# Performance work log

Measured on AMD Instinct MI355X. Metric: run time of the kernel, lower is better.

The kernel has to match this reference:

```python
import jax, jax.numpy as jnp
import numpy as np

N_BUCKET, EPB, K, TAU = 4, 4, 2, 1.0
C, H = 512, 1024
E = N_BUCKET * EPB
B, T = 2, 1024

def _l2norm(v):
    # matches F.normalize(dim=-1): v / max(||v||, 1e-12)
    return v / jnp.maximum(jnp.linalg.norm(v, axis=-1, keepdims=True), 1e-12)

def setup_inputs() -> dict:
    key = jax.random.key(0)
    ks = jax.random.split(key, 8)
    s = 1.0 / np.sqrt(C).astype(np.float32)
    sh = 1.0 / np.sqrt(H).astype(np.float32)
    return {
        "x": jax.random.normal(ks[0], (B, T, C), jnp.float32),
        "op_id": jax.random.randint(ks[1], (B, T), 0, N_BUCKET),
        "expert_key": jax.random.normal(ks[2], (N_BUCKET, EPB, C), jnp.float32) * s,
        "sW1": jax.random.normal(ks[3], (C, H), jnp.float32) * s,
        "sb1": jnp.zeros((H,), jnp.float32),
        "sW2": jax.random.normal(ks[4], (H, C), jnp.float32) * sh,
        "sb2": jnp.zeros((C,), jnp.float32),
        "eW1": jax.random.normal(ks[5], (E, C, H), jnp.float32) * s,
        "eb1": jnp.zeros((E, H), jnp.float32),
        "eW2": jax.random.normal(ks[6], (E, H, C), jnp.float32) * sh,
        "eb2": jnp.zeros((E, C), jnp.float32),
        "gate_logit": jnp.float32(-2.0),
    }

def reference(x, op_id, expert_key, sW1, sb1, sW2, sb2, eW1, eb1, eW2, eb2, gate_logit):
    Bb, Tt, Cc = x.shape
    # --- HierKVRouter ---
    bucket = jnp.clip(op_id, 0, N_BUCKET - 1)                 # (B,T)
    h_n = _l2norm(x)                                          # (B,T,C)
    keys = _l2norm(expert_key)                                # (nb,epb,C)
    keys_bt = keys[bucket]                                    # (B,T,epb,C) gather
    score = jnp.einsum('btc,btec->bte', h_n, keys_bt) / max(TAU, 1e-6)
    probs_local = jax.nn.softmax(score, axis=-1)              # (B,T,epb)
    topv, local = jax.lax.top_k(probs_local, K)               # (B,T,K)
    w = topv / (jnp.sum(topv, axis=-1, keepdims=True) + 1e-9) # combine weights
    gid = bucket[..., None] * EPB + local                     # (B,T,K) global ids
    # --- dispatch / expert MLP / combine ---
    flat_in = jnp.broadcast_to(x[:, :, None, :], (Bb, Tt, K, Cc)).reshape(-1, Cc)
    flat_gid = gid.reshape(-1)                                # (B*T*K,)
    flat_w = w.reshape(-1)                                    # (B*T*K,)
    out = jnp.zeros_like(flat_in)
    for e in range(E):  # fixed small expert count; masked dense = exact math of torch boolean-mask loop
        mask = (flat_gid == e)[:, None]
        h1 = jax.nn.relu(flat_in @ eW1[e] + eb1[e])
        oe = h1 @ eW2[e] + eb2[e]
        out = out + jnp.where(mask, oe * flat_w[:, None], 0.0)
    moe_out = out.reshape(Bb, Tt, K, Cc).sum(axis=2)          # (B,T,C)
    # --- shared dense FFN + gated combine ---
    dense = jax.nn.relu(x @ sW1 + sb1) @ sW2 + sb2
    y = dense + jax.nn.sigmoid(gate_logit) * moe_out
    return y
```

## Files before the change

### kernel.cpp

```cpp
#include <hip/hip_runtime.h>
#include <hip/hip_bf16.h>
#include <math.h>

#define C_DIM 512
#define H_DIM 1024
#define NTOK  2048
#define NSLOT 4096
#define NROWS 6144
#define MAXT128 64
#define MAXT64  112

typedef __attribute__((ext_vector_type(8))) short short8;
typedef __attribute__((ext_vector_type(4))) float floatx4;
typedef __attribute__((address_space(3))) void as3_void;
typedef const __attribute__((address_space(1))) void as1_cvoid;

__device__ __forceinline__ void gload_lds16(const void* g, void* l){
  __builtin_amdgcn_global_load_lds((as1_cvoid*)g, (as3_void*)l, 16, 0, 0);
}

__device__ __forceinline__ unsigned short f2b(float f){
  unsigned int u = __float_as_uint(f);
  unsigned int r = (u + 0x7FFFu + ((u >> 16) & 1u)) >> 16;
  return (unsigned short)r;
}

#define NB_CVT 1024
#define NB_RTR 512
#define NB_T1  2176
#define NB_T2  2176

__global__ __launch_bounds__(256) void k_prep(const float* __restrict__ x,
                                              const int* __restrict__ op_id,
                                              const float* __restrict__ ekey,
                                              const float* __restrict__ sW1,
                                              const float* __restrict__ sW2,
                                              const float* __restrict__ eW1,
                                              const float* __restrict__ eW2,
                                              unsigned short* __restrict__ Xb,
                                              unsigned short* __restrict__ sW1t,
                                              unsigned short* __restrict__ sW2t,
                                              unsigned short* __restrict__ eW1t,
                                              unsigned short* __restrict__ eW2t,
                                              int* __restrict__ gids,
                                              float* __restrict__ wv){
  __shared__ float tile[64 * 65];
  const int bid = blockIdx.x;
  const int tid = threadIdx.x;

  if (bid < NB_CVT){
    int i = bid * 256 + tid;
    float4 v = reinterpret_cast<const float4*>(x)[i];
    ushort4 o;
    o.x = f2b(v.x); o.y = f2b(v.y); o.z = f2b(v.z); o.w = f2b(v.w);
    reinterpret_cast<ushort4*>(Xb)[i] = o;
    return;
  }
  if (bid < NB_CVT + NB_RTR){
    int t = (bid - NB_CVT) * 4 + (tid >> 6);
    int lane = tid & 63;
    const float* xr = x + (size_t)t * C_DIM;
    float xs[8];
    float xn2 = 0.f;
    #pragma unroll
    for (int i = 0; i < 8; i++){ float v = xr[lane + 64*i]; xs[i] = v; xn2 += v*v; }
    #pragma unroll
    for (int o = 32; o; o >>= 1) xn2 += __shfl_xor(xn2, o, 64);
    int bucket = min(max(op_id[t], 0), 3);
    float xn = fmaxf(sqrtf(xn2), 1e-12f);
    float p[4];
    #pragma unroll
    for (int e = 0; e < 4; e++){
      const float* kr = ekey + ((size_t)bucket * 4 + e) * C_DIM;
      float dot = 0.f, kn2 = 0.f;
      #pragma unroll
      for (int i = 0; i < 8; i++){ float kv = kr[lane + 64*i]; dot += xs[i]*kv; kn2 += kv*kv; }
      #pragma unroll
      for (int o = 32; o; o >>= 1){ dot += __shfl_xor(dot, o, 64); kn2 += __shfl_xor(kn2, o, 64); }
      float kn = fmaxf(sqrtf(kn2), 1e-12f);
      p[e] = dot / (xn * kn);
    }
    float mx = fmaxf(fmaxf(p[0], p[1]), fmaxf(p[2], p[3]));
    float Z = 0.f;
    #pragma unroll
    for (int e = 0; e < 4; e++){ p[e] = expf(p[e] - mx); Z += p[e]; }
    #pragma unroll
    for (int e = 0; e < 4; e++) p[e] /= Z;
    int i0 = 0;
    #pragma unroll
    for (int e = 1; e < 4; e++) if (p[e] > p[i0]) i0 = e;
    int i1 = (i0 == 0) ? 1 : 0;
    #pragma unroll
    for (int e = 0; e < 4; e++) if (e != i0 && e != i1 && p[e] > p[i1]) i1 = e;
    float v0 = p[i0], v1 = p[i1];
    float wsum = v0 + v1 + 1e-9f;
    if (lane == 0){
      gids[2*t]   = bucket * 4 + i0;
      gids[2*t+1] = bucket * 4 + i1;
      wv[2*t]   = v0 / wsum;
      wv[2*t+1] = v1 / wsum;
    }
    return;
  }

  const float* in; unsigned short* out;
  int K, N, n0, k0;
  if (bid < NB_CVT + NB_RTR + NB_T1){
    int tb = bid - (NB_CVT + NB_RTR);
    int mat = tb >> 7, tl = tb & 127;
    K = C_DIM; N = H_DIM;
    in  = (mat < 16) ? eW1 + (size_t)mat * K * N : sW1;
    out = (mat < 16) ? eW1t + (size_t)mat * K * N : sW1t;
    n0 = (tl & 15) * 64; k0 = (tl >> 4) * 64;
  } else {
    int tb = bid - (NB_CVT + NB_RTR + NB_T1);
    int mat = tb >> 7, tl = tb & 127;
    K = H_DIM; N = C_DIM;
    in  = (mat < 16) ? eW2 + (size_t)mat * K * N : sW2;
    out = (mat < 16) ? eW2t + (size_t)mat * K * N : sW2t;
    n0 = (tl & 7) * 64; k0 = (tl >> 3) * 64;
  }
  {
    int tx = tid & 15, ty = tid >> 4;
    #pragma unroll
    for (int i = 0; i < 4; i++){
      int k = ty + 16 * i;
      float4 v = *reinterpret_cast<const float4*>(in + (size_t)(k0 + k) * N + n0 + tx * 4);
      tile[k * 65 + tx * 4 + 0] = v.x;
      tile[k * 65 + tx * 4 + 1] = v.y;
      tile[k * 65 + tx * 4 + 2] = v.z;
      tile[k * 65 + tx * 4 + 3] = v.w;
    }
    __syncthreads();
    #pragma unroll
    for (int i = 0; i < 4; i++){
      int n = ty + 16 * i;
      ushort4 o;
      o.x = f2b(tile[(4*tx + 0) * 65 + n]);
      o.y = f2b(tile[(4*tx + 1) * 65 + n]);
      o.z = f2b(tile[(4*tx + 2) * 65 + n]);
      o.w = f2b(tile[(4*tx + 3) * 65 + n]);
      *reinterpret_cast<ushort4*>(out + (size_t)(n0 + n) * K + k0 + 4 * tx) = o;
    }
  }
}

__global__ __launch_bounds__(256) void k_sort(const int* __restrict__ gids,
                                              const float* __restrict__ wv,
                                              const float* __restrict__ gate,
                                              int* __restrict__ rowTok,
                                              float* __restrict__ rowW,
                                              int* __restrict__ tiles128,
                                              int* __restrict__ tiles64){
  __shared__ int hist[256][16];
  __shared__ int off[17];
  int t = threadIdx.x;
  float sig = 1.f / (1.f + expf(-gate[0]));
  int h[16];
  #pragma unroll
  for (int e = 0; e < 16; e++) h[e] = 0;
  int base = t * 16;
  for (int s = 0; s < 16; s++){ int g = gids[base + s]; h[g]++; }
  #pragma unroll
  for (int e = 0; e < 16; e++) hist[t][e] = h[e];
  __syncthreads();
  if (t < 16){
    int run = 0;
    for (int i = 0; i < 256; i++){ int v = hist[i][t]; hist[i][t] = run; run += v; }
    off[t + 1] = run;
  }
  __syncthreads();
  if (t == 0){ off[0] = 0; for (int e = 0; e < 16; e++) off[e+1] += off[e]; }
  __syncthreads();
  #pragma unroll
  for (int e = 0; e < 16; e++) h[e] = hist[t][e];
  for (int s = 0; s < 16; s++){
    int slot = base + s;
    int g = gids[slot];
    int pos = off[g] + h[g]; h[g]++;
    rowTok[NTOK + pos] = slot >> 1;
    rowW[NTOK + pos] = sig * wv[slot];
  }
  for (int r = t; r < NTOK; r += 256){ rowTok[r] = r; rowW[r] = 1.0f; }
  __syncthreads();
  if (t == 0){
    int nt = 0;
    for (int r0 = 0; r0 < NTOK; r0 += 128){
      tiles128[nt*3] = r0; tiles128[nt*3+1] = 128; tiles128[nt*3+2] = 16; nt++;
    }
    for (int e = 0; e < 16; e++){
      int c = off[e+1] - off[e];
      for (int r0 = 0; r0 < c; r0 += 128){
        tiles128[nt*3] = NTOK + off[e] + r0;
        tiles128[nt*3+1] = min(128, c - r0);
        tiles128[nt*3+2] = e;
        nt++;
      }
    }
    for (int i = nt; i < MAXT128; i++){ tiles128[i*3] = 0; tiles128[i*3+1] = 0; tiles128[i*3+2] = 0; }
    nt = 0;
    for (int r0 = 0; r0 < NTOK; r0 += 64){
      tiles64[nt*3] = r0; tiles64[nt*3+1] = 64; tiles64[nt*3+2] = 16; nt++;
    }
    for (int e = 0; e < 16; e++){
      int c = off[e+1] - off[e];
      for (int r0 = 0; r0 < c; r0 += 64){
        tiles64[nt*3] = NTOK + off[e] + r0;
        tiles64[nt*3+1] = min(64, c - r0);
        tiles64[nt*3+2] = e;
        nt++;
      }
    }
    for (int i = nt; i < MAXT64; i++){ tiles64[i*3] = 0; tiles64[i*3+1] = 0; tiles64[i*3+2] = 0; }
  }
}

template<int BMT, int KDIM, int NDIM, bool RELU, bool ATOMICY, bool GATHER>
__global__ __launch_bounds__(256) void k_gemm(const unsigned short* __restrict__ A,
                                              const unsigned short* __restrict__ BtE,
                                              const unsigned short* __restrict__ BtS,
                                              const float* __restrict__ biasE,
                                              const float* __restrict__ biasS,
                                              const int* __restrict__ rowTok,
                                              const float* __restrict__ rowW,
                                              const int* __restrict__ tiles,
                                              unsigned short* __restrict__ outB,
                                              float* __restrict__ y){
  const int tileId = blockIdx.x;
  const int rows = tiles[tileId*3+1];
  if (rows == 0) return;
  const int row0 = tiles[tileId*3];
  const int eid  = tiles[tileId*3+2];
  const unsigned short* Bt = (eid < 16) ? (BtE + (size_t)eid * NDIM * KDIM) : BtS;
  const float* bias = (eid < 16) ? (biasE + eid * NDIM) : biasS;
  const int n0 = blockIdx.y * 128;

  constexpr int MREP = BMT / 32;
  constexpr int AISS = BMT * 8 / 256;
  constexpr int NLD  = AISS + 4;

  __shared__ __align__(16) unsigned short As[2][BMT * 64];
  __shared__ __align__(16) unsigned short Bs[2][128 * 64];

  const int tid = threadIdx.x;
  const int lane = tid & 63;
  const int wid = tid >> 6;
  const int wm = wid >> 1, wn = wid & 1;
  const int l15 = lane & 15, lhi = lane >> 4;

  int aRow[AISS], aOff[AISS];
  #pragma unroll
  for (int j = 0; j < AISS; j++){
    int c = j * 256 + tid;
    int i = c >> 3, op = c & 7;
    int o = op ^ (i & 7);
    int ie = min(i, rows - 1);
    aRow[j] = GATHER ? rowTok[row0 + ie] : (row0 + ie);
    aOff[j] = o * 8;
  }
  int bRow[4], bOff[4];
  #pragma unroll
  for (int j = 0; j < 4; j++){
    int c = j * 256 + tid;
    int i = c >> 3, op = c & 7;
    int o = op ^ (i & 7);
    bRow[j] = n0 + i;
    bOff[j] = o * 8;
  }

  auto STAGE = [&](int buf, int kt){
    #pragma unroll
    for (int j = 0; j < AISS; j++)
      gload_lds16(A + (size_t)aRow[j] * KDIM + kt * 64 + aOff[j],
                  (char*)&As[buf][0] + (j * 256 + tid) * 16);
    #pragma unroll
    for (int j = 0; j < 4; j++)
      gload_lds16(Bt + (size_t)bRow[j] * KDIM + kt * 64 + bOff[j],
                  (char*)&Bs[buf][0] + (j * 256 + tid) * 16);
  };

  floatx4 acc[MREP][4] = {};
  constexpr int NT = KDIM / 64;

  STAGE(0, 0);
  for (int kt = 0; kt < NT; ++kt){
    const int cur = kt & 1;
    if (kt + 1 < NT){
      STAGE(cur ^ 1, kt + 1);
      if constexpr (NLD == 8) asm volatile("s_waitcnt vmcnt(8)" ::: "memory");
      else                    asm volatile("s_waitcnt vmcnt(6)" ::: "memory");
    } else {
      asm volatile("s_waitcnt vmcnt(0)" ::: "memory");
    }
    __builtin_amdgcn_s_barrier();
    asm volatile("" ::: "memory");
    #pragma unroll
    for (int kk = 0; kk < 2; ++kk){
      short8 a[MREP], b[4];
      #pragma unroll
      for (int m = 0; m < MREP; m++){
        int r = wm * (BMT/2) + m * 16 + l15;
        a[m] = *reinterpret_cast<const short8*>(
            (char*)&As[cur][0] + r * 128 + ((kk * 64 + lhi * 16) ^ ((r & 7) << 4)));
      }
      #pragma unroll
      for (int n = 0; n < 4; n++){
        int r = wn * 64 + n * 16 + l15;
        b[n] = *reinterpret_cast<const short8*>(
            (char*)&Bs[cur][0] + r * 128 + ((kk * 64 + lhi * 16) ^ ((r & 7) << 4)));
      }
      #pragma unroll
      for (int m = 0; m < MREP; m++)
        #pragma unroll
        for (int n = 0; n < 4; n++)
          acc[m][n] = __builtin_amdgcn_mfma_f32_16x16x32_bf16(a[m], b[n], acc[m][n], 0, 0, 0);
    }
    asm volatile("" ::: "memory");
    __builtin_amdgcn_s_barrier();
  }

  #pragma unroll
  for (int m = 0; m < MREP; m++){
    #pragma unroll
    for (int n = 0; n < 4; n++){
      int gcol = n0 + wn * 64 + n * 16 + l15;
      float bv = bias[gcol];
      #pragma unroll
      for (int q = 0; q < 4; q++){
        int ri = wm * (BMT/2) + m * 16 + lhi * 4 + q;
        if (ri < rows){
          float v = acc[m][n][q] + bv;
          if constexpr (ATOMICY){
            int tok = rowTok[row0 + ri];
            atomicAdd(y + (size_t)tok * NDIM + gcol, v * rowW[row0 + ri]);
          } else {
            if (RELU) v = fmaxf(v, 0.f);
            outB[(size_t)(row0 + ri) * NDIM + gcol] = f2b(v);
          }
        }
      }
    }
  }
}

extern "C" void kernel_launch(void* const* d_in, const int* in_sizes, int n_in,
                              void* d_out, int out_size, void* d_ws, size_t ws_size,
                              hipStream_t stream){
  const float* x    = (const float*)d_in[0];
  const int*   opid = (const int*)d_in[1];
  const float* ekey = (const float*)d_in[2];
  const float* sW1  = (const float*)d_in[3];
  const float* sb1  = (const float*)d_in[4];
  const float* sW2  = (const float*)d_in[5];
  const float* sb2  = (const float*)d_in[6];
  const float* eW1  = (const float*)d_in[7];
  const float* eb1  = (const float*)d_in[8];
  const float* eW2  = (const float*)d_in[9];
  const float* eb2  = (const float*)d_in[10];
  const float* gate = (const float*)d_in[11];
  float* y = (float*)d_out;

  char* ws = (char*)d_ws;
  size_t off = 0;
  auto alloc = [&](size_t bytes) -> char* {
    char* p = ws + off; off += (bytes + 255) & ~(size_t)255; return p;
  };
  unsigned short* Xb   = (unsigned short*)alloc((size_t)NTOK * C_DIM * 2);
  unsigned short* sW1t = (unsigned short*)alloc((size_t)H_DIM * C_DIM * 2);
  unsigned short* sW2t = (unsigned short*)alloc((size_t)C_DIM * H_DIM * 2);
  unsigned short* eW1t = (unsigned short*)alloc((size_t)16 * H_DIM * C_DIM * 2);
  unsigned short* eW2t = (unsigned short*)alloc((size_t)16 * C_DIM * H_DIM * 2);
  unsigned short* H1   = (unsigned short*)alloc((size_t)NROWS * H_DIM * 2);
  float* wv     = (float*)alloc((size_t)NSLOT * 4);
  int*   gids   = (int*)alloc((size_t)NSLOT * 4);
  int*   rowTok = (int*)alloc((size_t)NROWS * 4);
  float* rowW   = (float*)alloc((size_t)NROWS * 4);
  int*   tiles128 = (int*)alloc((size_t)MAXT128 * 3 * 4);
  int*   tiles64  = (int*)alloc((size_t)MAXT64 * 3 * 4);

  hipMemsetAsync(y, 0, (size_t)out_size * 4, stream);
  k_prep<<<NB_CVT + NB_RTR + NB_T1 + NB_T2, 256, 0, stream>>>(
      x, opid, ekey, sW1, sW2, eW1, eW2, Xb, sW1t, sW2t, eW1t, eW2t, gids, wv);
  k_sort<<<1, 256, 0, stream>>>(gids, wv, gate, rowTok, rowW, tiles128, tiles64);
  k_gemm<128, C_DIM, H_DIM, true,  false, true ><<<dim3(MAXT128, H_DIM/128), 256, 0, stream>>>(
      Xb, eW1t, sW1t, eb1, sb1, rowTok, rowW, tiles128, H1, nullptr);
  k_gemm<64,  H_DIM, C_DIM, false, true,  false><<<dim3(MAXT64, C_DIM/128), 256, 0, stream>>>(
      H1, eW2t, sW2t, eb2, sb2, rowTok, rowW, tiles64, nullptr, y);
}
```

Measured before the change: 90.46 us.

## Replace atomic scatter with per-row output buffer and gather-combine kernel; widen transpose tiles

The second GEMM now writes weighted per-row fp32 results to a dense buffer instead of doing atomicAdd into y, and a new combine kernel gathers the dense row and the two expert rows for each token via an inverse permutation recorded in the sort kernel. This removes the output memset and the contended atomics, but adds a 12 MB intermediate write plus read and an extra launch. Separately, the weight transpose in the prep kernel handles 64x128 tiles per block, with the LDS layout changed so the read-out uses float4 loads and each thread writes longer contiguous rows.

```diff
diff --git a/kernel.cpp b/kernel.cpp
--- a/kernel.cpp
+++ b/kernel.cpp
@@ -27,8 +27,8 @@
 
 #define NB_CVT 1024
 #define NB_RTR 512
-#define NB_T1  2176
-#define NB_T2  2176
+#define NB_T1  1088
+#define NB_T2  1088
 
 __global__ __launch_bounds__(256) void k_prep(const float* __restrict__ x,
                                               const int* __restrict__ op_id,
@@ -44,7 +44,7 @@
                                               unsigned short* __restrict__ eW2t,
                                               int* __restrict__ gids,
                                               float* __restrict__ wv){
-  __shared__ float tile[64 * 65];
+  __shared__ float tile[64 * 129];
   const int bid = blockIdx.x;
   const int tid = threadIdx.x;
 
@@ -107,40 +107,39 @@
   int K, N, n0, k0;
   if (bid < NB_CVT + NB_RTR + NB_T1){
     int tb = bid - (NB_CVT + NB_RTR);
-    int mat = tb >> 7, tl = tb & 127;
+    int mat = tb >> 6, tl = tb & 63;
     K = C_DIM; N = H_DIM;
     in  = (mat < 16) ? eW1 + (size_t)mat * K * N : sW1;
     out = (mat < 16) ? eW1t + (size_t)mat * K * N : sW1t;
-    n0 = (tl & 15) * 64; k0 = (tl >> 4) * 64;
+    n0 = (tl & 15) * 64; k0 = (tl >> 4) * 128;
   } else {
     int tb = bid - (NB_CVT + NB_RTR + NB_T1);
-    int mat = tb >> 7, tl = tb & 127;
+    int mat = tb >> 6, tl = tb & 63;
     K = H_DIM; N = C_DIM;
     in  = (mat < 16) ? eW2 + (size_t)mat * K * N : sW2;
     out = (mat < 16) ? eW2t + (size_t)mat * K * N : sW2t;
-    n0 = (tl & 7) * 64; k0 = (tl >> 3) * 64;
+    n0 = (tl & 7) * 64; k0 = (tl >> 3) * 128;
   }
   {
     int tx = tid & 15, ty = tid >> 4;
     #pragma unroll
-    for (int i = 0; i < 4; i++){
+    for (int i = 0; i < 8; i++){
       int k = ty + 16 * i;
       float4 v = *reinterpret_cast<const float4*>(in + (size_t)(k0 + k) * N + n0 + tx * 4);
-      tile[k * 65 + tx * 4 + 0] = v.x;
-      tile[k * 65 + tx * 4 + 1] = v.y;
-      tile[k * 65 + tx * 4 + 2] = v.z;
-      tile[k * 65 + tx * 4 + 3] = v.w;
+      tile[(4*tx + 0) * 129 + k] = v.x;
+      tile[(4*tx + 1) * 129 + k] = v.y;
+      tile[(4*tx + 2) * 129 + k] = v.z;
+      tile[(4*tx + 3) * 129 + k] = v.w;
     }
     __syncthreads();
-    #pragma unroll
-    for (int i = 0; i < 4; i++){
-      int n = ty + 16 * i;
+    int wt = tid & 31, wr = tid >> 5;
+    #pragma unroll
+    for (int i = 0; i < 8; i++){
+      int n = wr + 8 * i;
+      float4 v = *reinterpret_cast<const float4*>(&tile[n * 129 + 4 * wt]);
       ushort4 o;
-      o.x = f2b(tile[(4*tx + 0) * 65 + n]);
-      o.y = f2b(tile[(4*tx + 1) * 65 + n]);
-      o.z = f2b(tile[(4*tx + 2) * 65 + n]);
-      o.w = f2b(tile[(4*tx + 3) * 65 + n]);
-      *reinterpret_cast<ushort4*>(out + (size_t)(n0 + n) * K + k0 + 4 * tx) = o;
+      o.x = f2b(v.x); o.y = f2b(v.y); o.z = f2b(v.z); o.w = f2b(v.w);
+      *reinterpret_cast<ushort4*>(out + (size_t)(n0 + n) * K + k0 + 4 * wt) = o;
     }
   }
 }
@@ -148,6 +147,7 @@
 __global__ __launch_bounds__(256) void k_sort(const int* __restrict__ gids,
                                               const float* __restrict__ wv,
                                               const float* __restrict__ gate,
+                                              int* __restrict__ inv,
                                               int* __restrict__ rowTok,
                                               float* __restrict__ rowW,
                                               int* __restrict__ tiles128,
@@ -178,6 +178,7 @@
     int slot = base + s;
     int g = gids[slot];
     int pos = off[g] + h[g]; h[g]++;
+    inv[slot] = pos;
     rowTok[NTOK + pos] = slot >> 1;
     rowW[NTOK + pos] = sig * wv[slot];
   }
@@ -215,7 +216,7 @@
   }
 }
 
-template<int BMT, int KDIM, int NDIM, bool RELU, bool ATOMICY, bool GATHER>
+template<int BMT, int KDIM, int NDIM, bool RELU, bool OUTBF, bool WEIGHTED, bool GATHER>
 __global__ __launch_bounds__(256) void k_gemm(const unsigned short* __restrict__ A,
                                               const unsigned short* __restrict__ BtE,
                                               const unsigned short* __restrict__ BtS,
@@ -225,7 +226,7 @@
                                               const float* __restrict__ rowW,
                                               const int* __restrict__ tiles,
                                               unsigned short* __restrict__ outB,
-                                              float* __restrict__ y){
+                                              float* __restrict__ outF){
   const int tileId = blockIdx.x;
   const int rows = tiles[tileId*3+1];
   if (rows == 0) return;
@@ -330,17 +331,35 @@
         int ri = wm * (BMT/2) + m * 16 + lhi * 4 + q;
         if (ri < rows){
           float v = acc[m][n][q] + bv;
-          if constexpr (ATOMICY){
-            int tok = rowTok[row0 + ri];
-            atomicAdd(y + (size_t)tok * NDIM + gcol, v * rowW[row0 + ri]);
-          } else {
+          if constexpr (OUTBF){
             if (RELU) v = fmaxf(v, 0.f);
             outB[(size_t)(row0 + ri) * NDIM + gcol] = f2b(v);
+          } else {
+            if constexpr (WEIGHTED) v *= rowW[row0 + ri];
+            outF[(size_t)(row0 + ri) * NDIM + gcol] = v;
           }
         }
       }
     }
   }
+}
+
+__global__ __launch_bounds__(256) void k_combine(const float* __restrict__ O,
+                                                 const int* __restrict__ inv,
+                                                 float* __restrict__ y){
+  int q = blockIdx.x * 256 + threadIdx.x;
+  int t = q >> 7, c4 = q & 127;
+  const float4* Of = reinterpret_cast<const float4*>(O);
+  float4 d  = Of[(size_t)t * 128 + c4];
+  int p0 = inv[2*t], p1 = inv[2*t+1];
+  float4 o0 = Of[(size_t)(NTOK + p0) * 128 + c4];
+  float4 o1 = Of[(size_t)(NTOK + p1) * 128 + c4];
+  float4 r;
+  r.x = d.x + o0.x + o1.x;
+  r.y = d.y + o0.y + o1.y;
+  r.z = d.z + o0.z + o1.z;
+  r.w = d.w + o0.w + o1.w;
+  reinterpret_cast<float4*>(y)[q] = r;
 }
 
 extern "C" void kernel_launch(void* const* d_in, const int* in_sizes, int n_in,
@@ -371,19 +390,21 @@
   unsigned short* eW1t = (unsigned short*)alloc((size_t)16 * H_DIM * C_DIM * 2);
   unsigned short* eW2t = (unsigned short*)alloc((size_t)16 * C_DIM * H_DIM * 2);
   unsigned short* H1   = (unsigned short*)alloc((size_t)NROWS * H_DIM * 2);
+  float* O      = (float*)alloc((size_t)NROWS * C_DIM * 4);
   float* wv     = (float*)alloc((size_t)NSLOT * 4);
   int*   gids   = (int*)alloc((size_t)NSLOT * 4);
+  int*   inv    = (int*)alloc((size_t)NSLOT * 4);
   int*   rowTok = (int*)alloc((size_t)NROWS * 4);
   float* rowW   = (float*)alloc((size_t)NROWS * 4);
   int*   tiles128 = (int*)alloc((size_t)MAXT128 * 3 * 4);
   int*   tiles64  = (int*)alloc((size_t)MAXT64 * 3 * 4);
 
-  hipMemsetAsync(y, 0, (size_t)out_size * 4, stream);
   k_prep<<<NB_CVT + NB_RTR + NB_T1 + NB_T2, 256, 0, stream>>>(
       x, opid, ekey, sW1, sW2, eW1, eW2, Xb, sW1t, sW2t, eW1t, eW2t, gids, wv);
-  k_sort<<<1, 256, 0, stream>>>(gids, wv, gate, rowTok, rowW, tiles128, tiles64);
-  k_gemm<128, C_DIM, H_DIM, true,  false, true ><<<dim3(MAXT128, H_DIM/128), 256, 0, stream>>>(
+  k_sort<<<1, 256, 0, stream>>>(gids, wv, gate, inv, rowTok, rowW, tiles128, tiles64);
+  k_gemm<128, C_DIM, H_DIM, true,  true,  false, true ><<<dim3(MAXT128, H_DIM/128), 256, 0, stream>>>(
       Xb, eW1t, sW1t, eb1, sb1, rowTok, rowW, tiles128, H1, nullptr);
-  k_gemm<64,  H_DIM, C_DIM, false, true,  false><<<dim3(MAXT64, C_DIM/128), 256, 0, stream>>>(
-      H1, eW2t, sW2t, eb2, sb2, rowTok, rowW, tiles64, nullptr, y);
-}
+  k_gemm<64,  H_DIM, C_DIM, false, false, true,  false><<<dim3(MAXT64, C_DIM/128), 256, 0, stream>>>(
+      H1, eW2t, sW2t, eb2, sb2, rowTok, rowW, tiles64, nullptr, O);
+  k_combine<<<1024, 256, 0, stream>>>(O, inv, y);
+}
```

Result: faster. 82.77 us (-8.5%).
